# Optimization experiments

Measured on AMD Instinct MI355X. Metric: run time of the kernel, lower is better.

## Reference

```python
import jax, jax.numpy as jnp
import numpy as np

H = 16   # num_attention_heads
G = 4    # num_gqa_groups
D = 64   # head_dim = hidden // H
HIDDEN = 1024
KV_DIM = HIDDEN // H * G  # 256
EPS = 1e-5


def setup_inputs() -> dict:
    key = jax.random.key(0)
    k0, k1, k2, k3 = jax.random.split(key, 4)
    x = jax.random.normal(k0, (8, 4096, HIDDEN), dtype=jnp.float32)
    query_weight = jax.random.normal(k1, (HIDDEN, HIDDEN), dtype=jnp.float32) * 0.02
    key_weight = jax.random.normal(k2, (KV_DIM, HIDDEN), dtype=jnp.float32) * 0.02
    value_weight = jax.random.normal(k3, (KV_DIM, HIDDEN), dtype=jnp.float32) * 0.02
    return {
        "x": x,
        "query_weight": query_weight,
        "key_weight": key_weight,
        "value_weight": value_weight,
        "query_bias": jnp.zeros((HIDDEN,), jnp.float32),
        "key_bias": jnp.zeros((KV_DIM,), jnp.float32),
        "value_bias": jnp.zeros((KV_DIM,), jnp.float32),
        "layer_norm_weight": jnp.ones((HIDDEN,), jnp.float32),
        "layer_norm_bias": jnp.zeros((HIDDEN,), jnp.float32),
    }


def reference(x, query_weight, key_weight, value_weight, query_bias, key_bias,
              value_bias, layer_norm_weight, layer_norm_bias):
    b, s, _ = x.shape
    # Shared LayerNorm (q is k is v path in apply_qkv_norm)
    mu = jnp.mean(x, axis=-1, keepdims=True)
    var = jnp.mean(jnp.square(x - mu), axis=-1, keepdims=True)
    xn = (x - mu) * jax.lax.rsqrt(var + EPS) * layer_norm_weight + layer_norm_bias
    # Q/K/V projections (F.linear: x @ W.T + b)
    q = xn @ query_weight.T + query_bias           # [b, s, H*D]
    k = xn @ key_weight.T + key_bias               # [b, s, G*1*D]
    v = xn @ value_weight.T + value_bias           # [b, s, G*1*D]
    # 'b s (h d) -> b h s d'
    q = q.reshape(b, s, H, D).transpose(0, 2, 1, 3)           # [b, H, s, D]
    # 'b s (g h d) -> b h (g s) d' with h = KV_DIM//(G*D) = 1
    def kv_rearrange(t):
        t = t.reshape(b, s, G, 1, D)                          # b s g h d
        t = t.transpose(0, 3, 2, 1, 4)                        # b h g s d
        return t.reshape(b, 1, G * s, D)                      # [b, 1, G*s, D]
    return q, kv_rearrange(k), kv_rearrange(v)
```

## Files before the change

### kernel.cpp

```cpp
#include <hip/hip_runtime.h>
#include <hip/hip_bf16.h>


#define HIDDEN 1024
#define NTOK   32768

typedef __bf16 bf16x8 __attribute__((ext_vector_type(8)));
typedef float  f32x4  __attribute__((ext_vector_type(4)));

#define GLOBAL_AS(p) ((const __attribute__((address_space(1))) void*)(p))
#define LDS_AS(p)    ((__attribute__((address_space(3))) void*)(p))

__device__ __forceinline__ unsigned short f2bf(float f) {
  union { float f; unsigned int i; } x; x.f = f;
  unsigned int r = x.i + 0x7FFFu + ((x.i >> 16) & 1u);
  return (unsigned short)(r >> 16);
}

__global__ __launch_bounds__(256) void ln_cvt_kernel(
    const float* __restrict__ x,
    const float* __restrict__ gamma,
    const float* __restrict__ beta,
    const float* __restrict__ wq,
    const float* __restrict__ wk,
    const float* __restrict__ wv,
    unsigned short* __restrict__ xn,
    unsigned short* __restrict__ wb) {
  const int bid = blockIdx.x;
  const int t   = threadIdx.x;
  if (bid < NTOK) {
    const size_t base = (size_t)bid * HIDDEN;
    const float4 v = ((const float4*)(x + base))[t];
    float s  = v.x + v.y + v.z + v.w;
    float s2 = v.x*v.x + v.y*v.y + v.z*v.z + v.w*v.w;
#pragma unroll
    for (int off = 32; off >= 1; off >>= 1) {
      s  += __shfl_xor(s,  off);
      s2 += __shfl_xor(s2, off);
    }
    __shared__ float red[8];
    const int w = t >> 6;
    if ((t & 63) == 0) { red[w] = s; red[4 + w] = s2; }
    __syncthreads();
    s  = red[0] + red[1] + red[2] + red[3];
    s2 = red[4] + red[5] + red[6] + red[7];
    const float mu   = s * (1.0f / HIDDEN);
    const float rstd = rsqrtf(s2 * (1.0f / HIDDEN) - mu * mu + 1e-5f);
    const float4 g  = ((const float4*)gamma)[t];
    const float4 bb = ((const float4*)beta)[t];
    ushort4 o;
    o.x = f2bf((v.x - mu) * rstd * g.x + bb.x);
    o.y = f2bf((v.y - mu) * rstd * g.y + bb.y);
    o.z = f2bf((v.z - mu) * rstd * g.z + bb.z);
    o.w = f2bf((v.w - mu) * rstd * g.w + bb.w);
    ((ushort4*)(xn + base))[t] = o;
  } else {
    const int b2 = bid - NTOK;
    const float* src;
    int off;
    if (b2 < 1024)      { src = wq; off = b2; }
    else if (b2 < 1280) { src = wk; off = b2 - 1024; }
    else                { src = wv; off = b2 - 1280; }
    const float4 v = ((const float4*)src)[off * 256 + t];
    ushort4 o;
    o.x = f2bf(v.x); o.y = f2bf(v.y); o.z = f2bf(v.z); o.w = f2bf(v.w);
    ((ushort4*)wb)[b2 * 256 + t] = o;
  }
}

__global__ __launch_bounds__(512, 2) void qkv_gemm(
    const unsigned short* __restrict__ xn,
    const unsigned short* __restrict__ wqb,
    const float* __restrict__ bq,
    const float* __restrict__ bk,
    const float* __restrict__ bv,
    float* __restrict__ out) {
  __shared__ unsigned short Alds[32768];
  __shared__ unsigned short Blds[32768];

  const int bid = blockIdx.x;
  const int swz = (bid & 7) * 96 + (bid >> 3);
  const int mt  = swz / 6;
  const int nt  = swz % 6;
  const int brow = mt * 256;

  const unsigned short* wbase; const float* biasptr;
  int segcol; size_t obase; int hg;
  if (nt < 4)       { wbase = wqb + (size_t)nt * 256 * HIDDEN;  biasptr = bq; segcol = nt * 256; obase = 0u;        hg = 16; }
  else if (nt == 4) { wbase = wqb + (size_t)1024 * HIDDEN;      biasptr = bk; segcol = 0;        obase = 33554432u; hg = 4;  }
  else              { wbase = wqb + (size_t)1280 * HIDDEN;      biasptr = bv; segcol = 0;        obase = 41943040u; hg = 4;  }

  const int t = threadIdx.x;
  const int w = t >> 6, lane = t & 63;
  const int wm = w >> 2, wn = w & 3;
  const int l15 = lane & 15, hi = lane >> 4;

  const int sr  = 2 * w * 16 + (lane >> 2);
  const int scg = ((lane & 3) ^ ((lane >> 3) & 3)) * 8;
  const unsigned short* aST = xn    + (size_t)(brow + sr) * HIDDEN + scg;
  const unsigned short* bST = wbase + (size_t)sr * HIDDEN + scg;
  const int ldsq = 2 * w * 512;

  const int rdx  = (hi ^ ((l15 >> 1) & 3)) * 8;
  const int rowA = wm * 128 + l15;
  const int rowB = wn * 64  + l15;

  f32x4 acc[8][4];
#pragma unroll
  for (int m = 0; m < 8; ++m)
#pragma unroll
    for (int n = 0; n < 4; ++n) acc[m][n] = (f32x4){0.f, 0.f, 0.f, 0.f};
  bf16x8 a0[4], a1[4], b0[4], b1[4];

#define STA(BUF, KK, KT) do {                                                   \
    unsigned short* _d = Alds + (BUF) * 16384 + (KK) * 8192 + ldsq;             \
    const unsigned short* _s = aST + (size_t)((KT) * 64 + (KK) * 32);           \
    __builtin_amdgcn_global_load_lds(GLOBAL_AS(_s), LDS_AS(_d), 16, 0, 0);      \
    __builtin_amdgcn_global_load_lds(GLOBAL_AS(_s + 16 * HIDDEN), LDS_AS(_d + 512), 16, 0, 0); \
  } while (0)
#define STB(BUF, KK, KT) do {                                                   \
    unsigned short* _d = Blds + (BUF) * 16384 + (KK) * 8192 + ldsq;             \
    const unsigned short* _s = bST + (size_t)((KT) * 64 + (KK) * 32);           \
    __builtin_amdgcn_global_load_lds(GLOBAL_AS(_s), LDS_AS(_d), 16, 0, 0);      \
    __builtin_amdgcn_global_load_lds(GLOBAL_AS(_s + 16 * HIDDEN), LDS_AS(_d + 512), 16, 0, 0); \
  } while (0)
#define RDA(SET, BUF, KK, MH) do { _Pragma("unroll")                            \
    for (int m = 0; m < 4; ++m)                                                 \
      SET[m] = *(const bf16x8*)(Alds + (BUF) * 16384 + (KK) * 8192 + (rowA + (MH) * 64 + m * 16) * 32 + rdx); \
  } while (0)
#define RDB(SET, BUF, KK) do { _Pragma("unroll")                                \
    for (int n = 0; n < 4; ++n)                                                 \
      SET[n] = *(const bf16x8*)(Blds + (BUF) * 16384 + (KK) * 8192 + (rowB + n * 16) * 32 + rdx); \
  } while (0)
#define PIN __builtin_amdgcn_sched_barrier(0)
#define MMX(ASET, BSET, MH) do {                                                \
    _Pragma("unroll") for (int m = 0; m < 4; ++m)                               \
      _Pragma("unroll") for (int n = 0; n < 4; ++n)                             \
        acc[(MH) * 4 + m][n] = __builtin_amdgcn_mfma_f32_16x16x32_bf16(ASET[m], BSET[n], acc[(MH) * 4 + m][n], 0, 0, 0); \
  } while (0)
#define ENDPH(VMN) do {                                                         \
    asm volatile("s_waitcnt lgkmcnt(0)" ::: "memory");                          \
    asm volatile("s_waitcnt vmcnt(" #VMN ")" ::: "memory");                     \
    __builtin_amdgcn_sched_barrier(0);                                          \
    __builtin_amdgcn_s_barrier();                                               \
    __builtin_amdgcn_sched_barrier(0);                                          \
  } while (0)

  STA(0, 0, 0); STB(0, 0, 0); STA(0, 1, 0); STB(0, 1, 0);
  STA(1, 0, 1); STB(1, 0, 1); STA(1, 1, 1); STB(1, 1, 1);
  asm volatile("s_waitcnt vmcnt(12)" ::: "memory");
  __builtin_amdgcn_sched_barrier(0);
  __builtin_amdgcn_s_barrier();
  __builtin_amdgcn_sched_barrier(0);
  RDA(a0, 0, 0, 0); RDB(b0, 0, 0);
  asm volatile("s_waitcnt lgkmcnt(0)" ::: "memory");
  __builtin_amdgcn_sched_barrier(0);
  __builtin_amdgcn_s_barrier();
  __builtin_amdgcn_sched_barrier(0);

  for (int i = 0; i < 7; ++i) {
    const int T = 2 * i;
     STB(0, 0, T + 2); RDA(a1, 0, 0, 1);                PIN; MMX(a0, b0, 0); ENDPH(10);
     STA(0, 0, T + 2); RDA(a0, 0, 1, 0); RDB(b1, 0, 1); PIN; MMX(a1, b0, 1); ENDPH(10);
     STB(0, 1, T + 2); RDA(a1, 0, 1, 1);                PIN; MMX(a0, b1, 0); ENDPH(10);
     STA(0, 1, T + 2); RDA(a0, 1, 0, 0); RDB(b0, 1, 0); PIN; MMX(a1, b1, 1); ENDPH(10);
     STB(1, 0, T + 3); RDA(a1, 1, 0, 1);                PIN; MMX(a0, b0, 0); ENDPH(10);
     STA(1, 0, T + 3); RDA(a0, 1, 1, 0); RDB(b1, 1, 1); PIN; MMX(a1, b0, 1); ENDPH(10);
     STB(1, 1, T + 3); RDA(a1, 1, 1, 1);                PIN; MMX(a0, b1, 0); ENDPH(10);
     STA(1, 1, T + 3); RDA(a0, 0, 0, 0); RDB(b0, 0, 0); PIN; MMX(a1, b1, 1); ENDPH(10);
  }
   RDA(a1, 0, 0, 1);                PIN; MMX(a0, b0, 0); ENDPH(8);
   RDA(a0, 0, 1, 0); RDB(b1, 0, 1); PIN; MMX(a1, b0, 1); ENDPH(6);
   RDA(a1, 0, 1, 1);                PIN; MMX(a0, b1, 0); ENDPH(4);
   RDA(a0, 1, 0, 0); RDB(b0, 1, 0); PIN; MMX(a1, b1, 1); ENDPH(2);
   RDA(a1, 1, 0, 1);                PIN; MMX(a0, b0, 0); ENDPH(0);
   RDA(a0, 1, 1, 0); RDB(b1, 1, 1); PIN; MMX(a1, b0, 1); ENDPH(0);
   RDA(a1, 1, 1, 1);                PIN; MMX(a0, b1, 0); ENDPH(0);
                                         MMX(a1, b1, 1);
  asm volatile("s_waitcnt lgkmcnt(0)" ::: "memory");

#undef STA
#undef STB
#undef RDA
#undef RDB
#undef MMX
#undef PIN
#undef ENDPH

  float* ep = (float*)Alds;
  const int epb = w * 1344;
  const int headcol = segcol + wn * 64;
  const int gidx = headcol >> 6;
  const int tok0 = brow + wm * 128;
  const int b_ = tok0 >> 12;
  float* wout = out + obase + (size_t)(b_ * hg + gidx) * 262144u
                    + (size_t)(tok0 & 4095) * 64u;
  float biasv[4];
#pragma unroll
  for (int n = 0; n < 4; ++n) biasv[n] = biasptr[headcol + n * 16 + l15];

#pragma unroll
  for (int m = 0; m < 8; ++m) {
#pragma unroll
    for (int n = 0; n < 4; ++n)
#pragma unroll
      for (int j = 0; j < 4; ++j)
        ep[epb + (hi * 4 + j) * 84 + n * 16 + l15] = acc[m][n][j] + biasv[n];
    asm volatile("s_waitcnt lgkmcnt(0)" ::: "memory");
#pragma unroll
    for (int it = 0; it < 4; ++it) {
      const int r = it * 4 + hi;
      const float4 v = *(const float4*)(ep + epb + r * 84 + l15 * 4);
      *(float4*)(wout + (size_t)(m * 16 + r) * 64 + l15 * 4) = v;
    }
  }
}

extern "C" void kernel_launch(void* const* d_in, const int* in_sizes, int n_in,
                              void* d_out, int out_size, void* d_ws, size_t ws_size,
                              hipStream_t stream) {
  const float* x  = (const float*)d_in[0];
  const float* wq = (const float*)d_in[1];
  const float* wk = (const float*)d_in[2];
  const float* wv = (const float*)d_in[3];
  const float* bq = (const float*)d_in[4];
  const float* bk = (const float*)d_in[5];
  const float* bv = (const float*)d_in[6];
  const float* g  = (const float*)d_in[7];
  const float* be = (const float*)d_in[8];
  float* out = (float*)d_out;

  unsigned short* xn = (unsigned short*)d_ws;
  unsigned short* wb = (unsigned short*)((char*)d_ws + (64u << 20));

  ln_cvt_kernel<<<NTOK + 1536, 256, 0, stream>>>(x, g, be, wq, wk, wv, xn, wb);
  qkv_gemm<<<768, 512, 0, stream>>>(xn, wb, bq, bk, bv, out);
}
```

Baseline: 169.3 us.

## Shrink GEMM tile to 128x128 with simple double-buffered K loop

Replaces the 256x256-tile, 512-thread GEMM and its hand-interleaved 8-phase software pipeline with a 128x128 tile, 256-thread block, and a simple double-buffered loop over K in chunks of 32. The block count rises from 768 to 3072, LDS drops to 32 KB per block, and the launch bound asks for four blocks per CU. This aims to raise occupancy and spread the work more evenly across CUs. In exchange, each block reuses less data, so global and LDS traffic per FLOP grows, and every iteration waits on vmcnt(0) plus a barrier, which may leave loads less hidden behind MFMA work.

```diff
diff --git a/kernel.cpp b/kernel.cpp
--- a/kernel.cpp
+++ b/kernel.cpp
@@ -68,130 +68,116 @@
   }
 }
 
-__global__ __launch_bounds__(512, 2) void qkv_gemm(
+__global__ __launch_bounds__(256, 4) void qkv_gemm(
     const unsigned short* __restrict__ xn,
     const unsigned short* __restrict__ wqb,
     const float* __restrict__ bq,
     const float* __restrict__ bk,
     const float* __restrict__ bv,
     float* __restrict__ out) {
-  __shared__ unsigned short Alds[32768];
-  __shared__ unsigned short Blds[32768];
+  __shared__ unsigned short lds[16384];
+  unsigned short* Alds = lds;
+  unsigned short* Blds = lds + 8192;
 
   const int bid = blockIdx.x;
-  const int swz = (bid & 7) * 96 + (bid >> 3);
-  const int mt  = swz / 6;
-  const int nt  = swz % 6;
-  const int brow = mt * 256;
+  const int swz = (bid & 7) * 384 + (bid >> 3);
+  const int mt  = swz / 12;
+  const int nt  = swz % 12;
+  const int brow = mt * 128;
 
   const unsigned short* wbase; const float* biasptr;
   int segcol; size_t obase; int hg;
-  if (nt < 4)       { wbase = wqb + (size_t)nt * 256 * HIDDEN;  biasptr = bq; segcol = nt * 256; obase = 0u;        hg = 16; }
-  else if (nt == 4) { wbase = wqb + (size_t)1024 * HIDDEN;      biasptr = bk; segcol = 0;        obase = 33554432u; hg = 4;  }
-  else              { wbase = wqb + (size_t)1280 * HIDDEN;      biasptr = bv; segcol = 0;        obase = 41943040u; hg = 4;  }
+  if (nt < 8)        { wbase = wqb + (size_t)nt * 128 * HIDDEN;            biasptr = bq; segcol = nt * 128;        obase = 0u;        hg = 16; }
+  else if (nt < 10)  { wbase = wqb + (size_t)(1024 + (nt - 8) * 128) * HIDDEN;  biasptr = bk; segcol = (nt - 8) * 128;  obase = 33554432u; hg = 4; }
+  else               { wbase = wqb + (size_t)(1280 + (nt - 10) * 128) * HIDDEN; biasptr = bv; segcol = (nt - 10) * 128; obase = 41943040u; hg = 4; }
 
   const int t = threadIdx.x;
   const int w = t >> 6, lane = t & 63;
-  const int wm = w >> 2, wn = w & 3;
+  const int wm = w >> 1, wn = w & 1;
   const int l15 = lane & 15, hi = lane >> 4;
 
-  const int sr  = 2 * w * 16 + (lane >> 2);
+  const int sr  = w * 32 + (lane >> 2);
   const int scg = ((lane & 3) ^ ((lane >> 3) & 3)) * 8;
   const unsigned short* aST = xn    + (size_t)(brow + sr) * HIDDEN + scg;
   const unsigned short* bST = wbase + (size_t)sr * HIDDEN + scg;
-  const int ldsq = 2 * w * 512;
+  const int ldsq = w * 1024;
 
   const int rdx  = (hi ^ ((l15 >> 1) & 3)) * 8;
-  const int rowA = wm * 128 + l15;
-  const int rowB = wn * 64  + l15;
-
-  f32x4 acc[8][4];
-#pragma unroll
-  for (int m = 0; m < 8; ++m)
+  const int rowA = wm * 64 + l15;
+  const int rowB = wn * 64 + l15;
+
+  f32x4 acc[4][4];
+#pragma unroll
+  for (int m = 0; m < 4; ++m)
 #pragma unroll
     for (int n = 0; n < 4; ++n) acc[m][n] = (f32x4){0.f, 0.f, 0.f, 0.f};
-  bf16x8 a0[4], a1[4], b0[4], b1[4];
-
-#define STA(BUF, KK, KT) do {                                                   \
-    unsigned short* _d = Alds + (BUF) * 16384 + (KK) * 8192 + ldsq;             \
-    const unsigned short* _s = aST + (size_t)((KT) * 64 + (KK) * 32);           \
+  bf16x8 a[4], b[4];
+
+#define STA(BUF, KT) do {                                                       \
+    unsigned short* _d = Alds + (BUF) * 4096 + ldsq;                            \
+    const unsigned short* _s = aST + (size_t)((KT) * 32);                       \
     __builtin_amdgcn_global_load_lds(GLOBAL_AS(_s), LDS_AS(_d), 16, 0, 0);      \
     __builtin_amdgcn_global_load_lds(GLOBAL_AS(_s + 16 * HIDDEN), LDS_AS(_d + 512), 16, 0, 0); \
   } while (0)
-#define STB(BUF, KK, KT) do {                                                   \
-    unsigned short* _d = Blds + (BUF) * 16384 + (KK) * 8192 + ldsq;             \
-    const unsigned short* _s = bST + (size_t)((KT) * 64 + (KK) * 32);           \
+#define STB(BUF, KT) do {                                                       \
+    unsigned short* _d = Blds + (BUF) * 4096 + ldsq;                            \
+    const unsigned short* _s = bST + (size_t)((KT) * 32);                       \
     __builtin_amdgcn_global_load_lds(GLOBAL_AS(_s), LDS_AS(_d), 16, 0, 0);      \
     __builtin_amdgcn_global_load_lds(GLOBAL_AS(_s + 16 * HIDDEN), LDS_AS(_d + 512), 16, 0, 0); \
   } while (0)
-#define RDA(SET, BUF, KK, MH) do { _Pragma("unroll")                            \
+#define RD(BUF) do { _Pragma("unroll")                                          \
     for (int m = 0; m < 4; ++m)                                                 \
-      SET[m] = *(const bf16x8*)(Alds + (BUF) * 16384 + (KK) * 8192 + (rowA + (MH) * 64 + m * 16) * 32 + rdx); \
-  } while (0)
-#define RDB(SET, BUF, KK) do { _Pragma("unroll")                                \
+      a[m] = *(const bf16x8*)(Alds + (BUF) * 4096 + (rowA + m * 16) * 32 + rdx);\
+    _Pragma("unroll")                                                           \
     for (int n = 0; n < 4; ++n)                                                 \
-      SET[n] = *(const bf16x8*)(Blds + (BUF) * 16384 + (KK) * 8192 + (rowB + n * 16) * 32 + rdx); \
+      b[n] = *(const bf16x8*)(Blds + (BUF) * 4096 + (rowB + n * 16) * 32 + rdx);\
+  } while (0)
+#define MMX do { _Pragma("unroll")                                              \
+    for (int m = 0; m < 4; ++m)                                                 \
+      _Pragma("unroll") for (int n = 0; n < 4; ++n)                             \
+        acc[m][n] = __builtin_amdgcn_mfma_f32_16x16x32_bf16(a[m], b[n], acc[m][n], 0, 0, 0); \
   } while (0)
 #define PIN __builtin_amdgcn_sched_barrier(0)
-#define MMX(ASET, BSET, MH) do {                                                \
-    _Pragma("unroll") for (int m = 0; m < 4; ++m)                               \
-      _Pragma("unroll") for (int n = 0; n < 4; ++n)                             \
-        acc[(MH) * 4 + m][n] = __builtin_amdgcn_mfma_f32_16x16x32_bf16(ASET[m], BSET[n], acc[(MH) * 4 + m][n], 0, 0, 0); \
-  } while (0)
-#define ENDPH(VMN) do {                                                         \
-    asm volatile("s_waitcnt lgkmcnt(0)" ::: "memory");                          \
-    asm volatile("s_waitcnt vmcnt(" #VMN ")" ::: "memory");                     \
-    __builtin_amdgcn_sched_barrier(0);                                          \
-    __builtin_amdgcn_s_barrier();                                               \
-    __builtin_amdgcn_sched_barrier(0);                                          \
-  } while (0)
-
-  STA(0, 0, 0); STB(0, 0, 0); STA(0, 1, 0); STB(0, 1, 0);
-  STA(1, 0, 1); STB(1, 0, 1); STA(1, 1, 1); STB(1, 1, 1);
-  asm volatile("s_waitcnt vmcnt(12)" ::: "memory");
-  __builtin_amdgcn_sched_barrier(0);
+
+  STA(0, 0); STB(0, 0);
+  asm volatile("s_waitcnt vmcnt(0)" ::: "memory");
+  PIN;
   __builtin_amdgcn_s_barrier();
-  __builtin_amdgcn_sched_barrier(0);
-  RDA(a0, 0, 0, 0); RDB(b0, 0, 0);
+  PIN;
+
+#pragma unroll 2
+  for (int T = 0; T < 31; ++T) {
+    const int buf = T & 1;
+    RD(buf);
+    STA(buf ^ 1, T + 1);
+    STB(buf ^ 1, T + 1);
+    PIN;
+    asm volatile("s_waitcnt lgkmcnt(0)" ::: "memory");
+    PIN;
+    MMX;
+    asm volatile("s_waitcnt vmcnt(0)" ::: "memory");
+    PIN;
+    __builtin_amdgcn_s_barrier();
+    PIN;
+  }
+  RD(1);
   asm volatile("s_waitcnt lgkmcnt(0)" ::: "memory");
-  __builtin_amdgcn_sched_barrier(0);
+  PIN;
+  MMX;
   __builtin_amdgcn_s_barrier();
-  __builtin_amdgcn_sched_barrier(0);
-
-  for (int i = 0; i < 7; ++i) {
-    const int T = 2 * i;
-     STB(0, 0, T + 2); RDA(a1, 0, 0, 1);                PIN; MMX(a0, b0, 0); ENDPH(10);
-     STA(0, 0, T + 2); RDA(a0, 0, 1, 0); RDB(b1, 0, 1); PIN; MMX(a1, b0, 1); ENDPH(10);
-     STB(0, 1, T + 2); RDA(a1, 0, 1, 1);                PIN; MMX(a0, b1, 0); ENDPH(10);
-     STA(0, 1, T + 2); RDA(a0, 1, 0, 0); RDB(b0, 1, 0); PIN; MMX(a1, b1, 1); ENDPH(10);
-     STB(1, 0, T + 3); RDA(a1, 1, 0, 1);                PIN; MMX(a0, b0, 0); ENDPH(10);
-     STA(1, 0, T + 3); RDA(a0, 1, 1, 0); RDB(b1, 1, 1); PIN; MMX(a1, b0, 1); ENDPH(10);
-     STB(1, 1, T + 3); RDA(a1, 1, 1, 1);                PIN; MMX(a0, b1, 0); ENDPH(10);
-     STA(1, 1, T + 3); RDA(a0, 0, 0, 0); RDB(b0, 0, 0); PIN; MMX(a1, b1, 1); ENDPH(10);
-  }
-   RDA(a1, 0, 0, 1);                PIN; MMX(a0, b0, 0); ENDPH(8);
-   RDA(a0, 0, 1, 0); RDB(b1, 0, 1); PIN; MMX(a1, b0, 1); ENDPH(6);
-   RDA(a1, 0, 1, 1);                PIN; MMX(a0, b1, 0); ENDPH(4);
-   RDA(a0, 1, 0, 0); RDB(b0, 1, 0); PIN; MMX(a1, b1, 1); ENDPH(2);
-   RDA(a1, 1, 0, 1);                PIN; MMX(a0, b0, 0); ENDPH(0);
-   RDA(a0, 1, 1, 0); RDB(b1, 1, 1); PIN; MMX(a1, b0, 1); ENDPH(0);
-   RDA(a1, 1, 1, 1);                PIN; MMX(a0, b1, 0); ENDPH(0);
-                                         MMX(a1, b1, 1);
-  asm volatile("s_waitcnt lgkmcnt(0)" ::: "memory");
+  PIN;
 
 #undef STA
 #undef STB
-#undef RDA
-#undef RDB
+#undef RD
 #undef MMX
 #undef PIN
-#undef ENDPH
-
-  float* ep = (float*)Alds;
+
+  float* ep = (float*)lds;
   const int epb = w * 1344;
   const int headcol = segcol + wn * 64;
   const int gidx = headcol >> 6;
-  const int tok0 = brow + wm * 128;
+  const int tok0 = brow + wm * 64;
   const int b_ = tok0 >> 12;
   float* wout = out + obase + (size_t)(b_ * hg + gidx) * 262144u
                     + (size_t)(tok0 & 4095) * 64u;
@@ -200,7 +186,7 @@
   for (int n = 0; n < 4; ++n) biasv[n] = biasptr[headcol + n * 16 + l15];
 
 #pragma unroll
-  for (int m = 0; m < 8; ++m) {
+  for (int m = 0; m < 4; ++m) {
 #pragma unroll
     for (int n = 0; n < 4; ++n)
 #pragma unroll
@@ -234,5 +220,5 @@
   unsigned short* wb = (unsigned short*)((char*)d_ws + (64u << 20));
 
   ln_cvt_kernel<<<NTOK + 1536, 256, 0, stream>>>(x, g, be, wq, wk, wv, xn, wb);
-  qkv_gemm<<<768, 512, 0, stream>>>(xn, wb, bq, bk, bv, out);
-}
+  qkv_gemm<<<3072, 256, 0, stream>>>(xn, wb, bq, bk, bv, out);
+}
```

New measurement: 186.0 us. 9.9% more time.

## Use 4-wave blocks with 128x128 warp tiles and triple-buffered K=32 stages

Applied to the files above, without the earlier changes.

Moves the QKV GEMM from 8 waves per 256x256 tile to 4 waves, each computing a 128x128 sub-tile with 64 accumulators. The K loop now uses 32-wide slices in a three-stage rotating LDS buffer in place of the double buffer with split halves, which cuts barrier phases per MFMA. The intent is more register-level reuse of A and B fragments and fewer LDS reads per flop. In exchange there are fewer waves to hide latency, higher register pressure at one block per CU, and an epilogue rewritten to scatter per-row float4 writes.

```diff
diff --git a/kernel.cpp b/kernel.cpp
--- a/kernel.cpp
+++ b/kernel.cpp
@@ -68,15 +68,15 @@
   }
 }
 
-__global__ __launch_bounds__(512, 2) void qkv_gemm(
+__global__ __launch_bounds__(256, 1) void qkv_gemm(
     const unsigned short* __restrict__ xn,
     const unsigned short* __restrict__ wqb,
     const float* __restrict__ bq,
     const float* __restrict__ bk,
     const float* __restrict__ bv,
     float* __restrict__ out) {
-  __shared__ unsigned short Alds[32768];
-  __shared__ unsigned short Blds[32768];
+  __shared__ unsigned short Alds[24576];
+  __shared__ unsigned short Blds[24576];
 
   const int bid = blockIdx.x;
   const int swz = (bid & 7) * 96 + (bid >> 3);
@@ -92,128 +92,110 @@
 
   const int t = threadIdx.x;
   const int w = t >> 6, lane = t & 63;
-  const int wm = w >> 2, wn = w & 3;
+  const int wm = w >> 1, wn = w & 1;
   const int l15 = lane & 15, hi = lane >> 4;
 
-  const int sr  = 2 * w * 16 + (lane >> 2);
+  const int sr  = w * 64 + (lane >> 2);
   const int scg = ((lane & 3) ^ ((lane >> 3) & 3)) * 8;
   const unsigned short* aST = xn    + (size_t)(brow + sr) * HIDDEN + scg;
   const unsigned short* bST = wbase + (size_t)sr * HIDDEN + scg;
-  const int ldsq = 2 * w * 512;
+  const int ldsq = w * 2048;
 
   const int rdx  = (hi ^ ((l15 >> 1) & 3)) * 8;
   const int rowA = wm * 128 + l15;
-  const int rowB = wn * 64  + l15;
-
-  f32x4 acc[8][4];
+  const int rowB = wn * 128 + l15;
+
+  f32x4 acc[8][8];
 #pragma unroll
   for (int m = 0; m < 8; ++m)
 #pragma unroll
-    for (int n = 0; n < 4; ++n) acc[m][n] = (f32x4){0.f, 0.f, 0.f, 0.f};
-  bf16x8 a0[4], a1[4], b0[4], b1[4];
-
-#define STA(BUF, KK, KT) do {                                                   \
-    unsigned short* _d = Alds + (BUF) * 16384 + (KK) * 8192 + ldsq;             \
-    const unsigned short* _s = aST + (size_t)((KT) * 64 + (KK) * 32);           \
-    __builtin_amdgcn_global_load_lds(GLOBAL_AS(_s), LDS_AS(_d), 16, 0, 0);      \
-    __builtin_amdgcn_global_load_lds(GLOBAL_AS(_s + 16 * HIDDEN), LDS_AS(_d + 512), 16, 0, 0); \
-  } while (0)
-#define STB(BUF, KK, KT) do {                                                   \
-    unsigned short* _d = Blds + (BUF) * 16384 + (KK) * 8192 + ldsq;             \
-    const unsigned short* _s = bST + (size_t)((KT) * 64 + (KK) * 32);           \
-    __builtin_amdgcn_global_load_lds(GLOBAL_AS(_s), LDS_AS(_d), 16, 0, 0);      \
-    __builtin_amdgcn_global_load_lds(GLOBAL_AS(_s + 16 * HIDDEN), LDS_AS(_d + 512), 16, 0, 0); \
-  } while (0)
-#define RDA(SET, BUF, KK, MH) do { _Pragma("unroll")                            \
-    for (int m = 0; m < 4; ++m)                                                 \
-      SET[m] = *(const bf16x8*)(Alds + (BUF) * 16384 + (KK) * 8192 + (rowA + (MH) * 64 + m * 16) * 32 + rdx); \
-  } while (0)
-#define RDB(SET, BUF, KK) do { _Pragma("unroll")                                \
-    for (int n = 0; n < 4; ++n)                                                 \
-      SET[n] = *(const bf16x8*)(Blds + (BUF) * 16384 + (KK) * 8192 + (rowB + n * 16) * 32 + rdx); \
+    for (int n = 0; n < 8; ++n) acc[m][n] = (f32x4){0.f, 0.f, 0.f, 0.f};
+  bf16x8 a0[8], b0[8], a1[8], b1[8];
+
+#define ST(BUFO, KT) do { _Pragma("unroll")                                     \
+    for (int i = 0; i < 4; ++i) {                                               \
+      __builtin_amdgcn_global_load_lds(                                         \
+          GLOBAL_AS(aST + (size_t)(KT) * 32 + (size_t)i * 16 * HIDDEN),         \
+          LDS_AS(Alds + (BUFO) + ldsq + i * 512), 16, 0, 0);                    \
+      __builtin_amdgcn_global_load_lds(                                         \
+          GLOBAL_AS(bST + (size_t)(KT) * 32 + (size_t)i * 16 * HIDDEN),         \
+          LDS_AS(Blds + (BUFO) + ldsq + i * 512), 16, 0, 0);                    \
+    }                                                                           \
+  } while (0)
+#define RD(SA, SB, BUFO) do { _Pragma("unroll")                                 \
+    for (int m = 0; m < 8; ++m)                                                 \
+      SA[m] = *(const bf16x8*)(Alds + (BUFO) + (rowA + m * 16) * 32 + rdx);     \
+    _Pragma("unroll")                                                           \
+    for (int n = 0; n < 8; ++n)                                                 \
+      SB[n] = *(const bf16x8*)(Blds + (BUFO) + (rowB + n * 16) * 32 + rdx);     \
+  } while (0)
+#define MMX(SA, SB) do { _Pragma("unroll")                                      \
+    for (int m = 0; m < 8; ++m)                                                 \
+      _Pragma("unroll") for (int n = 0; n < 8; ++n)                             \
+        acc[m][n] = __builtin_amdgcn_mfma_f32_16x16x32_bf16(SA[m], SB[n], acc[m][n], 0, 0, 0); \
   } while (0)
 #define PIN __builtin_amdgcn_sched_barrier(0)
-#define MMX(ASET, BSET, MH) do {                                                \
-    _Pragma("unroll") for (int m = 0; m < 4; ++m)                               \
-      _Pragma("unroll") for (int n = 0; n < 4; ++n)                             \
-        acc[(MH) * 4 + m][n] = __builtin_amdgcn_mfma_f32_16x16x32_bf16(ASET[m], BSET[n], acc[(MH) * 4 + m][n], 0, 0, 0); \
-  } while (0)
 #define ENDPH(VMN) do {                                                         \
     asm volatile("s_waitcnt lgkmcnt(0)" ::: "memory");                          \
     asm volatile("s_waitcnt vmcnt(" #VMN ")" ::: "memory");                     \
-    __builtin_amdgcn_sched_barrier(0);                                          \
-    __builtin_amdgcn_s_barrier();                                               \
-    __builtin_amdgcn_sched_barrier(0);                                          \
-  } while (0)
-
-  STA(0, 0, 0); STB(0, 0, 0); STA(0, 1, 0); STB(0, 1, 0);
-  STA(1, 0, 1); STB(1, 0, 1); STA(1, 1, 1); STB(1, 1, 1);
-  asm volatile("s_waitcnt vmcnt(12)" ::: "memory");
-  __builtin_amdgcn_sched_barrier(0);
-  __builtin_amdgcn_s_barrier();
-  __builtin_amdgcn_sched_barrier(0);
-  RDA(a0, 0, 0, 0); RDB(b0, 0, 0);
+    PIN; __builtin_amdgcn_s_barrier(); PIN;                                     \
+  } while (0)
+
+  ST(0, 0); ST(8192, 1); ST(16384, 2);
+  asm volatile("s_waitcnt vmcnt(16)" ::: "memory");
+  PIN; __builtin_amdgcn_s_barrier(); PIN;
+  RD(a0, b0, 0);
   asm volatile("s_waitcnt lgkmcnt(0)" ::: "memory");
-  __builtin_amdgcn_sched_barrier(0);
-  __builtin_amdgcn_s_barrier();
-  __builtin_amdgcn_sched_barrier(0);
-
-  for (int i = 0; i < 7; ++i) {
-    const int T = 2 * i;
-     STB(0, 0, T + 2); RDA(a1, 0, 0, 1);                PIN; MMX(a0, b0, 0); ENDPH(10);
-     STA(0, 0, T + 2); RDA(a0, 0, 1, 0); RDB(b1, 0, 1); PIN; MMX(a1, b0, 1); ENDPH(10);
-     STB(0, 1, T + 2); RDA(a1, 0, 1, 1);                PIN; MMX(a0, b1, 0); ENDPH(10);
-     STA(0, 1, T + 2); RDA(a0, 1, 0, 0); RDB(b0, 1, 0); PIN; MMX(a1, b1, 1); ENDPH(10);
-     STB(1, 0, T + 3); RDA(a1, 1, 0, 1);                PIN; MMX(a0, b0, 0); ENDPH(10);
-     STA(1, 0, T + 3); RDA(a0, 1, 1, 0); RDB(b1, 1, 1); PIN; MMX(a1, b0, 1); ENDPH(10);
-     STB(1, 1, T + 3); RDA(a1, 1, 1, 1);                PIN; MMX(a0, b1, 0); ENDPH(10);
-     STA(1, 1, T + 3); RDA(a0, 0, 0, 0); RDB(b0, 0, 0); PIN; MMX(a1, b1, 1); ENDPH(10);
+  PIN; __builtin_amdgcn_s_barrier(); PIN;
+
+  for (int T = 0; T < 28; T += 2) {
+    const int bS0 = (T % 3) * 8192, bR0 = ((T + 1) % 3) * 8192;
+    ST(bS0, T + 3); RD(a1, b1, bR0); PIN; MMX(a0, b0); ENDPH(8);
+    const int bS1 = ((T + 1) % 3) * 8192, bR1 = ((T + 2) % 3) * 8192;
+    ST(bS1, T + 4); RD(a0, b0, bR1); PIN; MMX(a1, b1); ENDPH(8);
   }
-   RDA(a1, 0, 0, 1);                PIN; MMX(a0, b0, 0); ENDPH(8);
-   RDA(a0, 0, 1, 0); RDB(b1, 0, 1); PIN; MMX(a1, b0, 1); ENDPH(6);
-   RDA(a1, 0, 1, 1);                PIN; MMX(a0, b1, 0); ENDPH(4);
-   RDA(a0, 1, 0, 0); RDB(b0, 1, 0); PIN; MMX(a1, b1, 1); ENDPH(2);
-   RDA(a1, 1, 0, 1);                PIN; MMX(a0, b0, 0); ENDPH(0);
-   RDA(a0, 1, 1, 0); RDB(b1, 1, 1); PIN; MMX(a1, b0, 1); ENDPH(0);
-   RDA(a1, 1, 1, 1);                PIN; MMX(a0, b1, 0); ENDPH(0);
-                                         MMX(a1, b1, 1);
+  ST(8192, 31); RD(a1, b1, 16384); PIN; MMX(a0, b0); ENDPH(8);
+  RD(a0, b0, 0);                   PIN; MMX(a1, b1); ENDPH(0);
+  RD(a1, b1, 8192);                PIN; MMX(a0, b0);
   asm volatile("s_waitcnt lgkmcnt(0)" ::: "memory");
-
-#undef STA
-#undef STB
-#undef RDA
-#undef RDB
+  PIN; __builtin_amdgcn_s_barrier(); PIN;
+  MMX(a1, b1);
+
+#undef ST
+#undef RD
 #undef MMX
-#undef PIN
 #undef ENDPH
 
   float* ep = (float*)Alds;
-  const int epb = w * 1344;
-  const int headcol = segcol + wn * 64;
-  const int gidx = headcol >> 6;
+  const int epb = w * 2112;
   const int tok0 = brow + wm * 128;
-  const int b_ = tok0 >> 12;
-  float* wout = out + obase + (size_t)(b_ * hg + gidx) * 262144u
-                    + (size_t)(tok0 & 4095) * 64u;
-  float biasv[4];
-#pragma unroll
-  for (int n = 0; n < 4; ++n) biasv[n] = biasptr[headcol + n * 16 + l15];
+  float biasv[8];
+#pragma unroll
+  for (int n = 0; n < 8; ++n) biasv[n] = biasptr[segcol + wn * 128 + n * 16 + l15];
 
 #pragma unroll
   for (int m = 0; m < 8; ++m) {
 #pragma unroll
-    for (int n = 0; n < 4; ++n)
+    for (int n = 0; n < 8; ++n)
 #pragma unroll
       for (int j = 0; j < 4; ++j)
-        ep[epb + (hi * 4 + j) * 84 + n * 16 + l15] = acc[m][n][j] + biasv[n];
+        ep[epb + (hi * 4 + j) * 132 + n * 16 + l15] = acc[m][n][j] + biasv[n];
     asm volatile("s_waitcnt lgkmcnt(0)" ::: "memory");
-#pragma unroll
-    for (int it = 0; it < 4; ++it) {
-      const int r = it * 4 + hi;
-      const float4 v = *(const float4*)(ep + epb + r * 84 + l15 * 4);
-      *(float4*)(wout + (size_t)(m * 16 + r) * 64 + l15 * 4) = v;
+    PIN;
+#pragma unroll
+    for (int pass = 0; pass < 8; ++pass) {
+      const int r = pass * 2 + (lane >> 5);
+      const int c = (lane & 31) * 4;
+      const float4 v = *(const float4*)(ep + epb + r * 132 + c);
+      const int ncol = segcol + wn * 128 + c;
+      const int g = ncol >> 6, d = ncol & 63;
+      const int token = tok0 + m * 16 + r;
+      const int b_ = token >> 12, s = token & 4095;
+      *(float4*)(out + obase + (size_t)(b_ * hg + g) * 262144u
+                     + (size_t)s * 64u + d) = v;
     }
   }
+#undef PIN
 }
 
 extern "C" void kernel_launch(void* const* d_in, const int* in_sizes, int n_in,
@@ -234,5 +216,5 @@
   unsigned short* wb = (unsigned short*)((char*)d_ws + (64u << 20));
 
   ln_cvt_kernel<<<NTOK + 1536, 256, 0, stream>>>(x, g, be, wq, wk, wv, xn, wb);
-  qkv_gemm<<<768, 512, 0, stream>>>(xn, wb, bq, bk, bv, out);
-}
+  qkv_gemm<<<768, 256, 0, stream>>>(xn, wb, bq, bk, bv, out);
+}
```

New measurement: 204.1 us. +20.6%, slower.

## Load A fragments directly from global into registers, stage only B in LDS

Applied to the files above, without the earlier changes.

The GEMM no longer stages the activation (A) tile through LDS. Each wave loads its 8 A fragments straight from global memory into registers, double-buffered across K steps of 32. Only the weight (B) tile is staged via global_load_lds, and the LDS footprint shrinks from 128KB to about 43KB. This removes the LDS write/read traffic for A and part of the barrier work, but the K step per barrier halves and the unswizzled, strided global A loads may coalesce poorly and raise register pressure.

```diff
diff --git a/kernel.cpp b/kernel.cpp
--- a/kernel.cpp
+++ b/kernel.cpp
@@ -75,8 +75,8 @@
     const float* __restrict__ bk,
     const float* __restrict__ bv,
     float* __restrict__ out) {
-  __shared__ unsigned short Alds[32768];
-  __shared__ unsigned short Blds[32768];
+  __shared__ unsigned short lds[21600];
+  unsigned short* Blds = lds;
 
   const int bid = blockIdx.x;
   const int swz = (bid & 7) * 96 + (bid >> 3);
@@ -97,97 +97,68 @@
 
   const int sr  = 2 * w * 16 + (lane >> 2);
   const int scg = ((lane & 3) ^ ((lane >> 3) & 3)) * 8;
-  const unsigned short* aST = xn    + (size_t)(brow + sr) * HIDDEN + scg;
   const unsigned short* bST = wbase + (size_t)sr * HIDDEN + scg;
   const int ldsq = 2 * w * 512;
 
   const int rdx  = (hi ^ ((l15 >> 1) & 3)) * 8;
-  const int rowA = wm * 128 + l15;
-  const int rowB = wn * 64  + l15;
+  const int rowB = wn * 64 + l15;
+
+  const unsigned short* aP = xn + (size_t)(brow + wm * 128 + l15) * HIDDEN + hi * 8;
 
   f32x4 acc[8][4];
 #pragma unroll
   for (int m = 0; m < 8; ++m)
 #pragma unroll
     for (int n = 0; n < 4; ++n) acc[m][n] = (f32x4){0.f, 0.f, 0.f, 0.f};
-  bf16x8 a0[4], a1[4], b0[4], b1[4];
-
-#define STA(BUF, KK, KT) do {                                                   \
-    unsigned short* _d = Alds + (BUF) * 16384 + (KK) * 8192 + ldsq;             \
-    const unsigned short* _s = aST + (size_t)((KT) * 64 + (KK) * 32);           \
+  bf16x8 a0[8], a1[8], b[4];
+
+#define LDA(SET, KT) do { _Pragma("unroll")                                     \
+    for (int m = 0; m < 8; ++m)                                                 \
+      SET[m] = *(const bf16x8*)(aP + (size_t)m * 16 * HIDDEN + (KT) * 32);      \
+  } while (0)
+#define STB(BUF, KT) do {                                                       \
+    unsigned short* _d = Blds + (BUF) * 8192 + ldsq;                            \
+    const unsigned short* _s = bST + (size_t)((KT) * 32);                       \
     __builtin_amdgcn_global_load_lds(GLOBAL_AS(_s), LDS_AS(_d), 16, 0, 0);      \
     __builtin_amdgcn_global_load_lds(GLOBAL_AS(_s + 16 * HIDDEN), LDS_AS(_d + 512), 16, 0, 0); \
   } while (0)
-#define STB(BUF, KK, KT) do {                                                   \
-    unsigned short* _d = Blds + (BUF) * 16384 + (KK) * 8192 + ldsq;             \
-    const unsigned short* _s = bST + (size_t)((KT) * 64 + (KK) * 32);           \
-    __builtin_amdgcn_global_load_lds(GLOBAL_AS(_s), LDS_AS(_d), 16, 0, 0);      \
-    __builtin_amdgcn_global_load_lds(GLOBAL_AS(_s + 16 * HIDDEN), LDS_AS(_d + 512), 16, 0, 0); \
-  } while (0)
-#define RDA(SET, BUF, KK, MH) do { _Pragma("unroll")                            \
-    for (int m = 0; m < 4; ++m)                                                 \
-      SET[m] = *(const bf16x8*)(Alds + (BUF) * 16384 + (KK) * 8192 + (rowA + (MH) * 64 + m * 16) * 32 + rdx); \
-  } while (0)
-#define RDB(SET, BUF, KK) do { _Pragma("unroll")                                \
+#define RDB(BUF) do { _Pragma("unroll")                                         \
     for (int n = 0; n < 4; ++n)                                                 \
-      SET[n] = *(const bf16x8*)(Blds + (BUF) * 16384 + (KK) * 8192 + (rowB + n * 16) * 32 + rdx); \
+      b[n] = *(const bf16x8*)(Blds + (BUF) * 8192 + (rowB + n * 16) * 32 + rdx);\
+  } while (0)
+#define MMX(SA) do { _Pragma("unroll")                                          \
+    for (int m = 0; m < 8; ++m)                                                 \
+      _Pragma("unroll") for (int n = 0; n < 4; ++n)                             \
+        acc[m][n] = __builtin_amdgcn_mfma_f32_16x16x32_bf16(SA[m], b[n], acc[m][n], 0, 0, 0); \
   } while (0)
 #define PIN __builtin_amdgcn_sched_barrier(0)
-#define MMX(ASET, BSET, MH) do {                                                \
-    _Pragma("unroll") for (int m = 0; m < 4; ++m)                               \
-      _Pragma("unroll") for (int n = 0; n < 4; ++n)                             \
-        acc[(MH) * 4 + m][n] = __builtin_amdgcn_mfma_f32_16x16x32_bf16(ASET[m], BSET[n], acc[(MH) * 4 + m][n], 0, 0, 0); \
-  } while (0)
-#define ENDPH(VMN) do {                                                         \
-    asm volatile("s_waitcnt lgkmcnt(0)" ::: "memory");                          \
-    asm volatile("s_waitcnt vmcnt(" #VMN ")" ::: "memory");                     \
-    __builtin_amdgcn_sched_barrier(0);                                          \
-    __builtin_amdgcn_s_barrier();                                               \
-    __builtin_amdgcn_sched_barrier(0);                                          \
-  } while (0)
-
-  STA(0, 0, 0); STB(0, 0, 0); STA(0, 1, 0); STB(0, 1, 0);
-  STA(1, 0, 1); STB(1, 0, 1); STA(1, 1, 1); STB(1, 1, 1);
-  asm volatile("s_waitcnt vmcnt(12)" ::: "memory");
-  __builtin_amdgcn_sched_barrier(0);
-  __builtin_amdgcn_s_barrier();
-  __builtin_amdgcn_sched_barrier(0);
-  RDA(a0, 0, 0, 0); RDB(b0, 0, 0);
-  asm volatile("s_waitcnt lgkmcnt(0)" ::: "memory");
-  __builtin_amdgcn_sched_barrier(0);
-  __builtin_amdgcn_s_barrier();
-  __builtin_amdgcn_sched_barrier(0);
-
-  for (int i = 0; i < 7; ++i) {
-    const int T = 2 * i;
-     STB(0, 0, T + 2); RDA(a1, 0, 0, 1);                PIN; MMX(a0, b0, 0); ENDPH(10);
-     STA(0, 0, T + 2); RDA(a0, 0, 1, 0); RDB(b1, 0, 1); PIN; MMX(a1, b0, 1); ENDPH(10);
-     STB(0, 1, T + 2); RDA(a1, 0, 1, 1);                PIN; MMX(a0, b1, 0); ENDPH(10);
-     STA(0, 1, T + 2); RDA(a0, 1, 0, 0); RDB(b0, 1, 0); PIN; MMX(a1, b1, 1); ENDPH(10);
-     STB(1, 0, T + 3); RDA(a1, 1, 0, 1);                PIN; MMX(a0, b0, 0); ENDPH(10);
-     STA(1, 0, T + 3); RDA(a0, 1, 1, 0); RDB(b1, 1, 1); PIN; MMX(a1, b0, 1); ENDPH(10);
-     STB(1, 1, T + 3); RDA(a1, 1, 1, 1);                PIN; MMX(a0, b1, 0); ENDPH(10);
-     STA(1, 1, T + 3); RDA(a0, 0, 0, 0); RDB(b0, 0, 0); PIN; MMX(a1, b1, 1); ENDPH(10);
+#define VMW(N) asm volatile("s_waitcnt vmcnt(" #N ")" ::: "memory")
+#define LGKM0 asm volatile("s_waitcnt lgkmcnt(0)" ::: "memory")
+#define BAR __builtin_amdgcn_s_barrier()
+
+  LDA(a0, 0); STB(0, 0);
+
+  for (int T = 0; T < 30; T += 2) {
+    LDA(a1, T + 1); STB(1, T + 1); PIN; VMW(10); PIN; BAR; PIN;
+    RDB(0); LGKM0; PIN; MMX(a0);
+    LDA(a0, T + 2); STB(0, T + 2); PIN; VMW(10); PIN; BAR; PIN;
+    RDB(1); LGKM0; PIN; MMX(a1);
   }
-   RDA(a1, 0, 0, 1);                PIN; MMX(a0, b0, 0); ENDPH(8);
-   RDA(a0, 0, 1, 0); RDB(b1, 0, 1); PIN; MMX(a1, b0, 1); ENDPH(6);
-   RDA(a1, 0, 1, 1);                PIN; MMX(a0, b1, 0); ENDPH(4);
-   RDA(a0, 1, 0, 0); RDB(b0, 1, 0); PIN; MMX(a1, b1, 1); ENDPH(2);
-   RDA(a1, 1, 0, 1);                PIN; MMX(a0, b0, 0); ENDPH(0);
-   RDA(a0, 1, 1, 0); RDB(b1, 1, 1); PIN; MMX(a1, b0, 1); ENDPH(0);
-   RDA(a1, 1, 1, 1);                PIN; MMX(a0, b1, 0); ENDPH(0);
-                                         MMX(a1, b1, 1);
-  asm volatile("s_waitcnt lgkmcnt(0)" ::: "memory");
-
-#undef STA
+  LDA(a1, 31); STB(1, 31); PIN; VMW(10); PIN; BAR; PIN;
+  RDB(0); LGKM0; PIN; MMX(a0);
+  VMW(0); PIN; BAR; PIN;
+  RDB(1); LGKM0; PIN; MMX(a1);
+  BAR;
+
+#undef LDA
 #undef STB
-#undef RDA
 #undef RDB
 #undef MMX
-#undef PIN
-#undef ENDPH
-
-  float* ep = (float*)Alds;
+#undef VMW
+#undef LGKM0
+#undef BAR
+
+  float* ep = (float*)lds;
   const int epb = w * 1344;
   const int headcol = segcol + wn * 64;
   const int gidx = headcol >> 6;
@@ -214,6 +185,7 @@
       *(float4*)(wout + (size_t)(m * 16 + r) * 64 + l15 * 4) = v;
     }
   }
+#undef PIN
 }
 
 extern "C" void kernel_launch(void* const* d_in, const int* in_sizes, int n_in,
```

After: 264.2 us. +56.1%, slower.
